# Optimization experiments

Hardware: AMD Instinct MI355X
Metric: run time of the kernel (lower is better)

The kernel has to match this reference:

```python
import jax, jax.numpy as jnp
import numpy as np

B, S, T, H, NH, NL = 16, 128, 64, 128, 8, 4
DH = H // NH
FF = 2 * H
SCALE = 1.0 / float(np.sqrt(DH))


def _ln(x, s, b):
    m = x.mean(-1, keepdims=True)
    v = ((x - m) ** 2).mean(-1, keepdims=True)
    return (x - m) * jax.lax.rsqrt(v + 1e-5) * s + b


def _block(x, mask, p):
    Wq, bq, Wk, bk, Wv, bv, Wo, bo, s1, c1, W1, d1, W2, d2, s2, c2 = p
    N, L, _ = x.shape
    q = (x @ Wq + bq).reshape(N, L, NH, DH)
    k = (x @ Wk + bk).reshape(N, L, NH, DH)
    v = (x @ Wv + bv).reshape(N, L, NH, DH)
    scores = jnp.einsum('nqhd,nkhd->nhqk', q, k) * SCALE
    scores = jnp.where(mask[:, None, :, :], scores, -1e9)
    a = jax.nn.softmax(scores, axis=-1)
    o = jnp.einsum('nhqk,nkhd->nqhd', a, v).reshape(N, L, H)
    x = _ln(x + o @ Wo + bo, s1, c1)
    h = jax.nn.relu(x @ W1 + d1)
    return _ln(x + h @ W2 + d2, s2, c2)


def setup_inputs():
    key = jax.random.key(0)
    ks = jax.random.split(key, 16)
    g = lambda k, shape: jax.random.normal(k, shape, jnp.float32) * 0.02
    return {
        'polylines': jax.random.normal(ks[0], (B, S, T, H), jnp.float32),
        'lengths': jax.random.randint(ks[1], (B, S), 0, T + 1),
        'proj_w': g(ks[2], (H, H)), 'proj_b': jnp.zeros((H,), jnp.float32),
        'proj_ln_s': jnp.ones((H,), jnp.float32), 'proj_ln_b': jnp.zeros((H,), jnp.float32),
        'pos_emb': g(ks[3], (1, T, H)),
        'Wq': g(ks[4], (NL, H, H)), 'bq': jnp.zeros((NL, H), jnp.float32),
        'Wk': g(ks[5], (NL, H, H)), 'bk': jnp.zeros((NL, H), jnp.float32),
        'Wv': g(ks[6], (NL, H, H)), 'bv': jnp.zeros((NL, H), jnp.float32),
        'Wo': g(ks[7], (NL, H, H)), 'bo': jnp.zeros((NL, H), jnp.float32),
        'ln1_s': jnp.ones((NL, H), jnp.float32), 'ln1_b': jnp.zeros((NL, H), jnp.float32),
        'W1': g(ks[8], (NL, H, FF)), 'b1': jnp.zeros((NL, FF), jnp.float32),
        'W2': g(ks[9], (NL, FF, H)), 'b2': jnp.zeros((NL, H), jnp.float32),
        'ln2_s': jnp.ones((NL, H), jnp.float32), 'ln2_b': jnp.zeros((NL, H), jnp.float32),
    }


def reference(polylines, lengths, proj_w, proj_b, proj_ln_s, proj_ln_b, pos_emb,
              Wq, bq, Wk, bk, Wv, bv, Wo, bo, ln1_s, ln1_b, W1, b1, W2, b2, ln2_s, ln2_b):
    # valid[b,s,t] = t < lengths[b,s]; lengths==0 -> polyline absent (fully padded)
    valid = jnp.arange(T)[None, None, :] < lengths[:, :, None]  # [B,S,T]
    x = jnp.where(valid[..., None], polylines, -1.0)            # -1 pad as in np.pad(constant_values=-1)
    # mask_temporal[b,s] = outer(valid[b,s], valid[b,s])
    mask_t = (valid[:, :, :, None] & valid[:, :, None, :]).reshape(B * S, T, T)
    # mask_spatial[b,t] = outer(valid[b,:,t], valid[b,:,t])
    vs = jnp.transpose(valid, (0, 2, 1))                        # [B,T,S]
    mask_s = (vs[:, :, :, None] & vs[:, :, None, :]).reshape(B * T, S, S)

    x = x.reshape(B * S, T, H)
    x = jax.nn.relu(_ln(x @ proj_w + proj_b, proj_ln_s, proj_ln_b))  # MLP: Linear->LN->ReLU
    x = x + pos_emb[:, :T, :]

    mask = mask_t
    for i in range(NL):
        if i == NL // 2:
            # switch from temporal to spatial attention: [B*S,T,H] -> [B*T,S,H]
            x = x.reshape(B, S, T, H).transpose(0, 2, 1, 3).reshape(B * T, S, H)
            mask = mask_s
        p = (Wq[i], bq[i], Wk[i], bk[i], Wv[i], bv[i], Wo[i], bo[i],
             ln1_s[i], ln1_b[i], W1[i], b1[i], W2[i], b2[i], ln2_s[i], ln2_b[i])
        x = _block(x, mask, p)
    # faithful to original final reshape (treats [B*T,S,H] buffer as [B,S,T,H])
    return x.reshape(B, S, T, H)[:, 0, :]
```

## Files before the change

kernel.cpp:

```cpp
#include <hip/hip_runtime.h>

typedef short short8 __attribute__((ext_vector_type(8)));
typedef short short4_t __attribute__((ext_vector_type(4)));
typedef float floatx4 __attribute__((ext_vector_type(4)));
typedef unsigned short ushort_t;

#define B_ 16
#define S_ 128
#define T_ 64
#define H_ 128
#define FF_ 256
#define SCALEQK 0.25f

#define EPI_BIAS 0
#define EPI_RELU 1
#define EPI_LNRES 2
#define EPI_PROJ 3

#define OFFP 0
#define OFFQ(l) (16384 + (l) * 65536)
#define OFFK(l) (OFFQ(l) + 16384)
#define OFFV(l) (OFFQ(l) + 32768)
#define OFFO(l) (OFFQ(l) + 49152)
#define OFFW1(l) (278528 + (l) * 65536)
#define OFFW2(l) (OFFW1(l) + 32768)

__device__ __forceinline__ float b2f(ushort_t u) {
    union { unsigned int i; float f; } x; x.i = ((unsigned int)u) << 16; return x.f;
}
__device__ __forceinline__ ushort_t f2b(float f) {
    union { float f; unsigned int i; } x; x.f = f;
    unsigned int r = x.i + 0x7fffu + ((x.i >> 16) & 1u);
    return (ushort_t)(r >> 16);
}
__device__ __forceinline__ int pack2b(float a, float b) {
    return (int)f2b(a) | ((int)f2b(b) << 16);
}

struct WtEnt { const float* src; int N; int K; int nclog2; int dstoff; };
struct WtArgs { WtEnt e[25]; };

__global__ __launch_bounds__(256) void wt_kernel(WtArgs a, ushort_t* __restrict__ dst) {
    WtEnt ent = a.e[blockIdx.x];
    const int tiles_c = ent.N >> 5;
    const int nt = (ent.K >> 5) * tiles_c;
    const int t = blockIdx.y;
    if (t >= nt) return;
    const int tc = t & (tiles_c - 1);
    const int tr = t >> ent.nclog2;
    __shared__ float ld[32 * 33];
    const int tid = threadIdx.x;
#pragma unroll
    for (int i = 0; i < 4; ++i) {
        int e = tid + i * 256;
        int rr = e >> 5, cc = e & 31;
        ld[rr * 33 + cc] = ent.src[(tr * 32 + rr) * ent.N + tc * 32 + cc];
    }
    __syncthreads();
    ushort_t* d = dst + ent.dstoff;
#pragma unroll
    for (int i = 0; i < 4; ++i) {
        int e = tid + i * 256;
        int rr = e >> 5, cc = e & 31;
        d[(tc * 32 + rr) * ent.K + tr * 32 + cc] = f2b(ld[cc * 33 + rr]);
    }
}

template<int K, int EPI, bool PAD, bool FINAL, bool MULTI, bool OUTB, bool AB16>
__global__ __launch_bounds__(256, 2) void gemm_mfma(
    const void* __restrict__ Av, int lda,
    const ushort_t* wt0, const ushort_t* wt1, const ushort_t* wt2,
    const float* b0, const float* b1, const float* b2,
    const float* __restrict__ resid, int rstride,
    const float* __restrict__ lns, const float* __restrict__ lnb,
    const float* __restrict__ pos, const int* __restrict__ lens,
    void* o0, void* o1, void* o2,
    int Ntot)
{
    __shared__ ushort_t aL[128 * 136];
    __shared__ ushort_t wL[128 * 136];

    const int tid = threadIdx.x;
    const int lane = tid & 63, wv = tid >> 6;
    const size_t rowbase = (size_t)blockIdx.x * 128;

    const ushort_t* wT; const float* bias; void* out; int cbase;
    if (MULTI) {
        int sel = blockIdx.y;
        wT = sel == 0 ? wt0 : (sel == 1 ? wt1 : wt2);
        bias = sel == 0 ? b0 : (sel == 1 ? b1 : b2);
        out = sel == 0 ? o0 : (sel == 1 ? o1 : o2);
        cbase = 0;
    } else {
        wT = wt0; bias = b0; out = o0; cbase = blockIdx.y * 128;
    }

    floatx4 acc[2][8];
#pragma unroll
    for (int a = 0; a < 2; ++a)
#pragma unroll
        for (int c = 0; c < 8; ++c) acc[a][c] = (floatx4){0.f, 0.f, 0.f, 0.f};

    const int arow = wv * 32 + (lane & 15);
    const int koff = (lane >> 4) * 8;

    for (int kc = 0; kc < K; kc += 128) {
        if (kc) __syncthreads();
#pragma unroll
        for (int it = 0; it < 8; ++it) {
            int e8 = tid + it * 256;
            int row = e8 >> 4, kg = e8 & 15;
            int kk = kc + kg * 8;
            short8 val;
            if (AB16) {
                val = *(const short8*)((const ushort_t*)Av + (size_t)(rowbase + row) * lda + kk);
            } else {
                const float* Af = (const float*)Av + (size_t)(rowbase + row) * lda + kk;
                float f[8];
                *(float4*)(f) = *(const float4*)(Af);
                *(float4*)(f + 4) = *(const float4*)(Af + 4);
                if (PAD) {
                    int r = (int)(rowbase + row);
                    if ((r & 63) >= lens[r >> 6]) {
#pragma unroll
                        for (int q = 0; q < 8; ++q) f[q] = -1.0f;
                    }
                }
#pragma unroll
                for (int q = 0; q < 8; ++q) val[q] = (short)f2b(f[q]);
            }
            *(short8*)&aL[row * 136 + kg * 8] = val;
        }
#pragma unroll
        for (int it = 0; it < 8; ++it) {
            int e8 = tid + it * 256;
            int n = e8 >> 4, kg = e8 & 15;
            *(short8*)&wL[n * 136 + kg * 8] =
                *(const short8*)&wT[(size_t)(cbase + n) * K + kc + kg * 8];
        }
        __syncthreads();
#pragma unroll
        for (int k0 = 0; k0 < 128; k0 += 32) {
            short8 a0 = *(const short8*)&aL[arow * 136 + k0 + koff];
            short8 a1 = *(const short8*)&aL[(arow + 16) * 136 + k0 + koff];
#pragma unroll
            for (int ct = 0; ct < 8; ++ct) {
                short8 b = *(const short8*)&wL[(ct * 16 + (lane & 15)) * 136 + k0 + koff];
                acc[0][ct] = __builtin_amdgcn_mfma_f32_16x16x32_bf16(a0, b, acc[0][ct], 0, 0, 0);
                acc[1][ct] = __builtin_amdgcn_mfma_f32_16x16x32_bf16(a1, b, acc[1][ct], 0, 0, 0);
            }
        }
    }

    const int col16 = lane & 15;
    const int rgrp = (lane >> 4) * 4;
    float bcol[8], lnsc[8], lnbc[8];
#pragma unroll
    for (int ct = 0; ct < 8; ++ct) bcol[ct] = bias[cbase + ct * 16 + col16];
    if (EPI == EPI_LNRES || EPI == EPI_PROJ) {
#pragma unroll
        for (int ct = 0; ct < 8; ++ct) {
            lnsc[ct] = lns[ct * 16 + col16];
            lnbc[ct] = lnb[ct * 16 + col16];
        }
    }

#pragma unroll
    for (int rt = 0; rt < 2; ++rt) {
        const int rbase = wv * 32 + rt * 16 + rgrp;
#pragma unroll
        for (int ct = 0; ct < 8; ++ct)
#pragma unroll
            for (int rg = 0; rg < 4; ++rg) {
                float v = acc[rt][ct][rg] + bcol[ct];
                if (EPI == EPI_LNRES)
                    v += resid[(rowbase + rbase + rg) * (size_t)rstride + ct * 16 + col16];
                acc[rt][ct][rg] = v;
            }
        if (EPI == EPI_LNRES || EPI == EPI_PROJ) {
            float mean[4], rstd[4];
#pragma unroll
            for (int rg = 0; rg < 4; ++rg) {
                float s = 0.f;
#pragma unroll
                for (int ct = 0; ct < 8; ++ct) s += acc[rt][ct][rg];
                s += __shfl_xor(s, 1); s += __shfl_xor(s, 2);
                s += __shfl_xor(s, 4); s += __shfl_xor(s, 8);
                mean[rg] = s * (1.f / 128.f);
            }
#pragma unroll
            for (int rg = 0; rg < 4; ++rg) {
                float s = 0.f;
#pragma unroll
                for (int ct = 0; ct < 8; ++ct) {
                    float d = acc[rt][ct][rg] - mean[rg];
                    s += d * d;
                }
                s += __shfl_xor(s, 1); s += __shfl_xor(s, 2);
                s += __shfl_xor(s, 4); s += __shfl_xor(s, 8);
                rstd[rg] = rsqrtf(s * (1.f / 128.f) + 1e-5f);
            }
#pragma unroll
            for (int ct = 0; ct < 8; ++ct)
#pragma unroll
                for (int rg = 0; rg < 4; ++rg)
                    acc[rt][ct][rg] = (acc[rt][ct][rg] - mean[rg]) * rstd[rg] * lnsc[ct] + lnbc[ct];
        }
#pragma unroll
        for (int ct = 0; ct < 8; ++ct)
#pragma unroll
            for (int rg = 0; rg < 4; ++rg) {
                size_t grow = rowbase + rbase + rg;
                int col = cbase + ct * 16 + col16;
                float v = acc[rt][ct][rg];
                if (EPI == EPI_RELU) v = fmaxf(v, 0.f);
                if (EPI == EPI_PROJ)
                    v = fmaxf(v, 0.f) + pos[((int)grow & 63) * H_ + ct * 16 + col16];
                if (FINAL) {
                    int b = (int)(grow >> 7), s = (int)(grow & 127);
                    if (s < T_) ((float*)out)[((size_t)(b * T_ + s)) * H_ + col] = v;
                } else if (OUTB) {
                    ((ushort_t*)out)[grow * (size_t)Ntot + col] = f2b(v);
                } else {
                    ((float*)out)[grow * (size_t)Ntot + col] = v;
                }
            }
    }
}

__global__ __launch_bounds__(256, 1) void attn_s(
    ushort_t* qo, const ushort_t* __restrict__ kk, const ushort_t* __restrict__ vv,
    const int* __restrict__ lens)
{
    __shared__ float kL[128 * 36];
    __shared__ float vL[128 * 36];
    __shared__ int vldL[128];
    const int tid = threadIdx.x;
    const int b = blockIdx.x, hp = blockIdx.y;
    const size_t rowg = (size_t)b * 128;

    if (tid < 128) vldL[tid] = (lens[b * 128 + tid] > 0) ? 1 : 0;
#pragma unroll
    for (int it = 0; it < 2; ++it) {
        int e8 = tid + it * 256;
        int j = e8 >> 2, dg = e8 & 3;
        short8 k8 = *(const short8*)&kk[(rowg + j) * 128 + hp * 32 + dg * 8];
        short8 v8 = *(const short8*)&vv[(rowg + j) * 128 + hp * 32 + dg * 8];
        float* kd = &kL[j * 36 + dg * 8];
        float* vd = &vL[j * 36 + dg * 8];
#pragma unroll
        for (int q = 0; q < 8; ++q) { kd[q] = b2f((ushort_t)k8[q]); vd[q] = b2f((ushort_t)v8[q]); }
    }
    __syncthreads();

    const int hl = tid >> 7;
    const int i = tid & 127;
    const int hc = hl * 16;
    const int h = hp * 2 + hl;

    float qf[16];
    {
        const short8* qp = (const short8*)&qo[(rowg + i) * 128 + h * 16];
        short8 q0 = qp[0], q1 = qp[1];
#pragma unroll
        for (int q = 0; q < 8; ++q) { qf[q] = b2f((ushort_t)q0[q]); qf[8 + q] = b2f((ushort_t)q1[q]); }
    }

    float sc[128];
    const bool iv = vldL[i] != 0;
#pragma unroll
    for (int j = 0; j < 128; ++j) {
        const float* kr = &kL[j * 36 + hc];
        float s = 0.f;
#pragma unroll
        for (int d = 0; d < 16; ++d) s = fmaf(qf[d], kr[d], s);
        sc[j] = (iv && vldL[j]) ? s * SCALEQK : -1e9f;
    }
    float m = -3.0e38f;
#pragma unroll
    for (int j = 0; j < 128; ++j) m = fmaxf(m, sc[j]);
    float sum = 0.f;
#pragma unroll
    for (int j = 0; j < 128; ++j) { float e = __expf(sc[j] - m); sc[j] = e; sum += e; }
    const float inv = 1.0f / sum;
    float of[16];
#pragma unroll
    for (int d = 0; d < 16; ++d) of[d] = 0.f;
#pragma unroll
    for (int j = 0; j < 128; ++j) {
        float p = sc[j] * inv;
        const float* vr = &vL[j * 36 + hc];
#pragma unroll
        for (int d = 0; d < 16; ++d) of[d] = fmaf(p, vr[d], of[d]);
    }
    short8 o0v, o1v;
#pragma unroll
    for (int q = 0; q < 8; ++q) { o0v[q] = (short)f2b(of[q]); o1v[q] = (short)f2b(of[8 + q]); }
    short8* op = (short8*)&qo[(rowg + i) * 128 + h * 16];
    op[0] = o0v; op[1] = o1v;
}

template<int RT, int CT, int KK>
__device__ __forceinline__ void mm_g(const ushort_t* aL, int sa,
                                     const ushort_t* __restrict__ wT,
                                     int colbase, int lane, floatx4 (&acc)[RT][CT]) {
    const int l15 = lane & 15, lq8 = (lane >> 4) * 8;
#pragma unroll
    for (int r = 0; r < RT; ++r)
#pragma unroll
        for (int c = 0; c < CT; ++c) acc[r][c] = (floatx4){0.f, 0.f, 0.f, 0.f};
#pragma unroll
    for (int k0 = 0; k0 < KK; k0 += 32) {
        short8 b[CT];
#pragma unroll
        for (int c = 0; c < CT; ++c)
            b[c] = *(const short8*)&wT[(colbase + c * 16 + l15) * KK + k0 + lq8];
#pragma unroll
        for (int r = 0; r < RT; ++r) {
            short8 a = *(const short8*)&aL[(r * 16 + l15) * sa + k0 + lq8];
#pragma unroll
            for (int c = 0; c < CT; ++c)
                acc[r][c] = __builtin_amdgcn_mfma_f32_16x16x32_bf16(a, b[c], acc[r][c], 0, 0, 0);
        }
    }
}

template<int RT, int CT>
__device__ __forceinline__ void add_bias(floatx4 (&acc)[RT][CT], const float* b,
                                         int colbase, int l15) {
#pragma unroll
    for (int c = 0; c < CT; ++c) {
        float bc = b[colbase + c * 16 + l15];
#pragma unroll
        for (int r = 0; r < RT; ++r)
#pragma unroll
            for (int g = 0; g < 4; ++g) acc[r][c][g] += bc;
    }
}

template<int RT, int CT>
__device__ __forceinline__ void add_resid_reg(floatx4 (&acc)[RT][CT],
                                              const float (&res)[RT][CT][4]) {
#pragma unroll
    for (int r = 0; r < RT; ++r)
#pragma unroll
        for (int c = 0; c < CT; ++c)
#pragma unroll
            for (int g = 0; g < 4; ++g) acc[r][c][g] += res[r][c][g];
}
template<int RT, int CT>
__device__ __forceinline__ void save_resid(float (&res)[RT][CT][4],
                                           const floatx4 (&acc)[RT][CT]) {
#pragma unroll
    for (int r = 0; r < RT; ++r)
#pragma unroll
        for (int c = 0; c < CT; ++c)
#pragma unroll
            for (int g = 0; g < 4; ++g) res[r][c][g] = acc[r][c][g];
}

template<int RT, int CT>
__device__ __forceinline__ void st_n(const floatx4 (&acc)[RT][CT], ushort_t* dst, int stride,
                                     int colbase, int l15, int lq) {
#pragma unroll
    for (int r = 0; r < RT; ++r)
#pragma unroll
        for (int g = 0; g < 4; ++g) {
            int row = r * 16 + lq * 4 + g;
#pragma unroll
            for (int c = 0; c < CT; ++c)
                dst[row * stride + colbase + c * 16 + l15] = f2b(acc[r][c][g]);
        }
}

template<int RT, int CT>
__device__ __forceinline__ void st_t(const floatx4 (&acc)[RT][CT], ushort_t* dst, int stride,
                                     int colbase, int l15, int lq) {
#pragma unroll
    for (int r = 0; r < RT; ++r)
#pragma unroll
        for (int c = 0; c < CT; ++c) {
            int d = colbase + c * 16 + l15;
            short4_t p;
#pragma unroll
            for (int g = 0; g < 4; ++g) p[g] = (short)f2b(acc[r][c][g]);
            *(short4_t*)&dst[d * stride + r * 16 + lq * 4] = p;
        }
}

template<int RT, int CT>
__device__ __forceinline__ void ln_norm(floatx4 (&acc)[RT][CT], float* redL,
                                        const float* lns, const float* lnb,
                                        int colbase, int l15, int lq, int wv) {
#pragma unroll
    for (int r = 0; r < RT; ++r)
#pragma unroll
        for (int g = 0; g < 4; ++g) {
            float s = 0.f, q = 0.f;
#pragma unroll
            for (int c = 0; c < CT; ++c) { float v = acc[r][c][g]; s += v; q += v * v; }
            s += __shfl_xor(s, 1); s += __shfl_xor(s, 2); s += __shfl_xor(s, 4); s += __shfl_xor(s, 8);
            q += __shfl_xor(q, 1); q += __shfl_xor(q, 2); q += __shfl_xor(q, 4); q += __shfl_xor(q, 8);
            if (l15 == 0) {
                int row = r * 16 + lq * 4 + g;
                redL[row * 8 + wv] = s;
                redL[row * 8 + 4 + wv] = q;
            }
        }
    __syncthreads();
#pragma unroll
    for (int r = 0; r < RT; ++r)
#pragma unroll
        for (int g = 0; g < 4; ++g) {
            int row = r * 16 + lq * 4 + g;
            float4 S = *(float4*)&redL[row * 8];
            float4 Q = *(float4*)&redL[row * 8 + 4];
            float mean = (S.x + S.y + S.z + S.w) * (1.f / 128.f);
            float var = (Q.x + Q.y + Q.z + Q.w) * (1.f / 128.f) - mean * mean;
            float rstd = rsqrtf(var + 1e-5f);
#pragma unroll
            for (int c = 0; c < CT; ++c) {
                int col = colbase + c * 16 + l15;
                acc[r][c][g] = (acc[r][c][g] - mean) * rstd * lns[col] + lnb[col];
            }
        }
}

template<int JT>
__device__ __forceinline__ void softmax_pack(floatx4 (&st)[JT], bool iv, unsigned jm,
                                             int (&px)[JT][2]) {
    float ev[JT][4];
    float mx = -3.0e38f;
#pragma unroll
    for (int jt = 0; jt < JT; ++jt)
#pragma unroll
        for (int g = 0; g < 4; ++g) {
            bool ok = iv && ((jm >> (jt * 4 + g)) & 1u);
            float s = ok ? st[jt][g] * SCALEQK : -1e9f;
            ev[jt][g] = s; mx = fmaxf(mx, s);
        }
    mx = fmaxf(mx, __shfl_xor(mx, 16)); mx = fmaxf(mx, __shfl_xor(mx, 32));
    float sum = 0.f;
#pragma unroll
    for (int jt = 0; jt < JT; ++jt)
#pragma unroll
        for (int g = 0; g < 4; ++g) { float e = __expf(ev[jt][g] - mx); ev[jt][g] = e; sum += e; }
    sum += __shfl_xor(sum, 16); sum += __shfl_xor(sum, 32);
    float inv = 1.f / sum;
#pragma unroll
    for (int jt = 0; jt < JT; ++jt) {
        px[jt][0] = pack2b(ev[jt][0] * inv, ev[jt][1] * inv);
        px[jt][1] = pack2b(ev[jt][2] * inv, ev[jt][3] * inv);
    }
}

__device__ __forceinline__ short8 pfrag(const int (*px)[2], int jc, int lq, int l15) {
    const int jA = (lq & 1) * 32 + l15;
    int a0 = __shfl(px[jc * 2][0], jA);
    int a1 = __shfl(px[jc * 2][1], jA);
    int a2 = __shfl(px[jc * 2][0], jA + 16);
    int a3 = __shfl(px[jc * 2][1], jA + 16);
    int b0 = __shfl(px[jc * 2 + 1][0], jA);
    int b1 = __shfl(px[jc * 2 + 1][1], jA);
    int b2 = __shfl(px[jc * 2 + 1][0], jA + 16);
    int b3 = __shfl(px[jc * 2 + 1][1], jA + 16);
    const bool t = (lq >> 1) != 0;
    union { int4 i; short8 s; } u;
    u.i = make_int4(t ? b0 : a0, t ? b1 : a1, t ? b2 : a2, t ? b3 : a3);
    return u.s;
}
__device__ __forceinline__ short8 vfrag(const ushort_t* vT, int stride, int row, int off) {
    int2 a = *(const int2*)&vT[row * stride + off];
    int2 b = *(const int2*)&vT[row * stride + off + 4];
    union { int4 i; short8 s; } u;
    u.i = make_int4(a.x, a.y, b.x, b.y);
    return u.s;
}

__global__ __launch_bounds__(256, 2) void k1_mega(
    const float* __restrict__ poly, const int* __restrict__ lens,
    const ushort_t* __restrict__ wt,
    const float* __restrict__ projb, const float* __restrict__ pls,
    const float* __restrict__ plb, const float* __restrict__ pos,
    const float* __restrict__ bq0, const float* __restrict__ bk0,
    const float* __restrict__ bv0, const float* __restrict__ bo0,
    const float* __restrict__ l1s0, const float* __restrict__ l1b0,
    const float* __restrict__ b10, const float* __restrict__ b20,
    const float* __restrict__ l2s0, const float* __restrict__ l2b0,
    const float* __restrict__ bq1, const float* __restrict__ bk1,
    const float* __restrict__ bv1,
    ushort_t* __restrict__ o1, float* __restrict__ xr0f)
{
    __shared__ ushort_t pool[34816];
    __shared__ float redL[512];
    __shared__ float psL[8 * 68];
    __shared__ float q1L[128];
    ushort_t* xL = pool;
    ushort_t* qL = pool + 8704;
    ushort_t* kL = pool + 17408;
    ushort_t* vT = pool + 26112;
    ushort_t* hL = pool + 17408;

    const int tid = threadIdx.x, lane = tid & 63, wv = tid >> 6;
    const int l15 = lane & 15, lq = lane >> 4;
    const int gid = blockIdx.x;
    const int len = lens[gid];

    {
        const float* pg = poly + (size_t)gid * 8192;
#pragma unroll
        for (int it = 0; it < 8; ++it) {
            int e4 = (tid + it * 256) * 4;
            int row = e4 >> 7, col = e4 & 127;
            float4 f = *(const float4*)(pg + e4);
            if (row >= len) { f.x = -1.f; f.y = -1.f; f.z = -1.f; f.w = -1.f; }
            short4_t u;
            u[0] = (short)f2b(f.x); u[1] = (short)f2b(f.y);
            u[2] = (short)f2b(f.z); u[3] = (short)f2b(f.w);
            *(short4_t*)&xL[row * 136 + col] = u;
        }
    }
    __syncthreads();

    floatx4 a2[4][2];
    float xre[4][2][4];

    mm_g<4, 2, 128>(xL, 136, wt + OFFP, wv * 32, lane, a2);
    add_bias<4, 2>(a2, projb, wv * 32, l15);
    ln_norm<4, 2>(a2, redL, pls, plb, wv * 32, l15, lq, wv);
    __syncthreads();
#pragma unroll
    for (int r = 0; r < 4; ++r)
#pragma unroll
        for (int gg = 0; gg < 4; ++gg) {
            int row = r * 16 + lq * 4 + gg;
#pragma unroll
            for (int c = 0; c < 2; ++c) {
                int col = wv * 32 + c * 16 + l15;
                float v = fmaxf(a2[r][c][gg], 0.f) + pos[row * 128 + col];
                xre[r][c][gg] = v;
                xL[row * 136 + col] = f2b(v);
            }
        }
    __syncthreads();

    mm_g<4, 2, 128>(xL, 136, wt + OFFQ(0), wv * 32, lane, a2);
    add_bias<4, 2>(a2, bq0, wv * 32, l15);
    st_n<4, 2>(a2, qL, 136, wv * 32, l15, lq);
    mm_g<4, 2, 128>(xL, 136, wt + OFFK(0), wv * 32, lane, a2);
    add_bias<4, 2>(a2, bk0, wv * 32, l15);
    st_n<4, 2>(a2, kL, 136, wv * 32, l15, lq);
    mm_g<4, 2, 128>(xL, 136, wt + OFFV(0), wv * 32, lane, a2);
    add_bias<4, 2>(a2, bv0, wv * 32, l15);
    st_t<4, 2>(a2, vT, 68, wv * 32, l15, lq);
    __syncthreads();

    {
        const int iRow = wv * 16 + l15;
        const bool iv = iRow < len;
        unsigned jm = 0;
#pragma unroll
        for (int jt = 0; jt < 4; ++jt)
#pragma unroll
            for (int gg = 0; gg < 4; ++gg)
                if (jt * 16 + lq * 4 + gg < len) jm |= (1u << (jt * 4 + gg));
        for (int h = 0; h < 8; ++h) {
            const int hc = h * 16;
            short8 z8 = {0, 0, 0, 0, 0, 0, 0, 0};
            short8 bqf = z8;
            if (lq < 2) bqf = *(const short8*)&qL[iRow * 136 + hc + lq * 8];
            floatx4 st[4];
#pragma unroll
            for (int jt = 0; jt < 4; ++jt) {
                short8 ak = z8;
                if (lq < 2) ak = *(const short8*)&kL[(jt * 16 + l15) * 136 + hc + lq * 8];
                floatx4 zz = {0.f, 0.f, 0.f, 0.f};
                st[jt] = __builtin_amdgcn_mfma_f32_16x16x32_bf16(ak, bqf, zz, 0, 0, 0);
            }
            int px[4][2];
            softmax_pack<4>(st, iv, jm, px);
            floatx4 ao = {0.f, 0.f, 0.f, 0.f};
#pragma unroll
            for (int jc = 0; jc < 2; ++jc) {
                short8 av = vfrag(vT, 68, hc + l15, jc * 32 + lq * 8);
                short8 bp = pfrag(px, jc, lq, l15);
                ao = __builtin_amdgcn_mfma_f32_16x16x32_bf16(av, bp, ao, 0, 0, 0);
            }
            short4_t w;
#pragma unroll
            for (int gg = 0; gg < 4; ++gg) w[gg] = (short)f2b(ao[gg]);
            *(short4_t*)&qL[iRow * 136 + hc + lq * 4] = w;
        }
    }
    __syncthreads();

    mm_g<4, 2, 128>(qL, 136, wt + OFFO(0), wv * 32, lane, a2);
    add_bias<4, 2>(a2, bo0, wv * 32, l15);
    add_resid_reg<4, 2>(a2, xre);
    ln_norm<4, 2>(a2, redL, l1s0, l1b0, wv * 32, l15, lq, wv);
    save_resid<4, 2>(xre, a2);
    st_n<4, 2>(a2, xL, 136, wv * 32, l15, lq);
    __syncthreads();

    {
        floatx4 a4[4][4];
        mm_g<4, 4, 128>(xL, 136, wt + OFFW1(0), wv * 64, lane, a4);
        add_bias<4, 4>(a4, b10, wv * 64, l15);
#pragma unroll
        for (int r = 0; r < 4; ++r)
#pragma unroll
            for (int c = 0; c < 4; ++c)
#pragma unroll
                for (int gg = 0; gg < 4; ++gg) a4[r][c][gg] = fmaxf(a4[r][c][gg], 0.f);
        st_n<4, 4>(a4, hL, 272, wv * 64, l15, lq);
    }
    __syncthreads();

    mm_g<4, 2, 256>(hL, 272, wt + OFFW2(0), wv * 32, lane, a2);
    add_bias<4, 2>(a2, b20, wv * 32, l15);
    add_resid_reg<4, 2>(a2, xre);
    ln_norm<4, 2>(a2, redL, l2s0, l2b0, wv * 32, l15, lq, wv);
    save_resid<4, 2>(xre, a2);
    st_n<4, 2>(a2, xL, 136, wv * 32, l15, lq);
    if (lq == 0) {
#pragma unroll
        for (int c = 0; c < 2; ++c)
            xr0f[(size_t)gid * 128 + wv * 32 + c * 16 + l15] = a2[0][c][0];
    }
    __syncthreads();

    mm_g<4, 2, 128>(xL, 136, wt + OFFK(1), wv * 32, lane, a2);
    add_bias<4, 2>(a2, bk1, wv * 32, l15);
    st_n<4, 2>(a2, kL, 136, wv * 32, l15, lq);
    mm_g<4, 2, 128>(xL, 136, wt + OFFV(1), wv * 32, lane, a2);
    add_bias<4, 2>(a2, bv1, wv * 32, l15);
    st_t<4, 2>(a2, vT, 68, wv * 32, l15, lq);
    if (tid < 128) {
        int d = tid;
        float a = bq1[d];
        const ushort_t* wq = wt + OFFQ(1) + d * 128;
#pragma unroll 4
        for (int j0 = 0; j0 < 128; j0 += 8) {
            short8 w8 = *(const short8*)&wq[j0];
            short8 x8 = *(const short8*)&xL[j0];
#pragma unroll
            for (int q = 0; q < 8; ++q)
                a = fmaf(b2f((ushort_t)x8[q]), b2f((ushort_t)w8[q]), a);
        }
        q1L[d] = a;
    }
    __syncthreads();

    {
        int h = tid >> 5, jj = tid & 31;
        int hc = h * 16;
        float s[2];
#pragma unroll
        for (int half = 0; half < 2; ++half) {
            int j = jj + half * 32;
            float a = 0.f;
            short8 k0v = *(const short8*)&kL[j * 136 + hc];
            short8 k1v = *(const short8*)&kL[j * 136 + hc + 8];
#pragma unroll
            for (int q = 0; q < 8; ++q) {
                a = fmaf(q1L[hc + q], b2f((ushort_t)k0v[q]), a);
                a = fmaf(q1L[hc + 8 + q], b2f((ushort_t)k1v[q]), a);
            }
            s[half] = (j < len) ? a * SCALEQK : -1e9f;
        }
        float mx = fmaxf(s[0], s[1]);
#pragma unroll
        for (int d = 1; d < 32; d <<= 1) mx = fmaxf(mx, __shfl_xor(mx, d));
        float e0 = __expf(s[0] - mx), e1 = __expf(s[1] - mx);
        float sum = e0 + e1;
#pragma unroll
        for (int d = 1; d < 32; d <<= 1) sum += __shfl_xor(sum, d);
        float inv = 1.f / sum;
        psL[h * 68 + jj] = e0 * inv;
        psL[h * 68 + jj + 32] = e1 * inv;
    }
    __syncthreads();
    if (tid < 128) {
        int h = tid >> 4, d = tid & 15, hc = h * 16;
        float a = 0.f;
#pragma unroll 4
        for (int j0 = 0; j0 < 64; j0 += 4) {
            float4 p4 = *(const float4*)&psL[h * 68 + j0];
            short4_t v4 = *(const short4_t*)&vT[(hc + d) * 68 + j0];
            a += p4.x * b2f((ushort_t)v4[0]) + p4.y * b2f((ushort_t)v4[1])
               + p4.z * b2f((ushort_t)v4[2]) + p4.w * b2f((ushort_t)v4[3]);
        }
        o1[(size_t)gid * 128 + hc + d] = f2b(a);
    }
}

extern "C" void kernel_launch(void* const* d_in, const int* in_sizes, int n_in,
                              void* d_out, int out_size, void* d_ws, size_t ws_size,
                              hipStream_t stream)
{
    const float* poly   = (const float*)d_in[0];
    const int*   lens   = (const int*)d_in[1];
    const float* proj_w = (const float*)d_in[2];
    const float* proj_b = (const float*)d_in[3];
    const float* pls    = (const float*)d_in[4];
    const float* plb    = (const float*)d_in[5];
    const float* pos    = (const float*)d_in[6];
    const float* Wq = (const float*)d_in[7];
    const float* bq = (const float*)d_in[8];
    const float* Wk = (const float*)d_in[9];
    const float* bk = (const float*)d_in[10];
    const float* Wv = (const float*)d_in[11];
    const float* bv = (const float*)d_in[12];
    const float* Wo = (const float*)d_in[13];
    const float* bo = (const float*)d_in[14];
    const float* l1s = (const float*)d_in[15];
    const float* l1b = (const float*)d_in[16];
    const float* W1 = (const float*)d_in[17];
    const float* b1 = (const float*)d_in[18];
    const float* W2 = (const float*)d_in[19];
    const float* b2 = (const float*)d_in[20];
    const float* l2s = (const float*)d_in[21];
    const float* l2b = (const float*)d_in[22];
    float* outp = (float*)d_out;

    char* base = (char*)d_ws;
    ushort_t* wt    = (ushort_t*)base;
    ushort_t* o1buf = (ushort_t*)(base + 1081344);
    float* xr0f     = (float*)(base + 1605632);
    float* ybuf     = (float*)(base + 2654208);
    ushort_t* hsml  = (ushort_t*)(base + 3702784);
    ushort_t* q2    = (ushort_t*)(base + 4751360);
    ushort_t* k2b   = (ushort_t*)(base + 5275648);
    ushort_t* v2    = (ushort_t*)(base + 5799936);

    const int HH = H_ * H_, HF = H_ * FF_;
    WtArgs wa;
    wa.e[0] = {proj_w, 128, 128, 2, OFFP};
    for (int l = 0; l < 4; ++l) {
        wa.e[1 + l * 4 + 0] = {Wq + l * HH, 128, 128, 2, OFFQ(l)};
        wa.e[1 + l * 4 + 1] = {Wk + l * HH, 128, 128, 2, OFFK(l)};
        wa.e[1 + l * 4 + 2] = {Wv + l * HH, 128, 128, 2, OFFV(l)};
        wa.e[1 + l * 4 + 3] = {Wo + l * HH, 128, 128, 2, OFFO(l)};
    }
    for (int l = 0; l < 4; ++l) {
        wa.e[17 + l * 2 + 0] = {W1 + l * HF, 256, 128, 3, OFFW1(l)};
        wa.e[17 + l * 2 + 1] = {W2 + l * HF, 128, 256, 2, OFFW2(l)};
    }
    wt_kernel<<<dim3(25, 32), 256, 0, stream>>>(wa, wt);

    k1_mega<<<dim3(2048), 256, 0, stream>>>(
        poly, lens, wt,
        proj_b, pls, plb, pos,
        bq, bk, bv, bo, l1s, l1b, b1, b2, l2s, l2b,
        bq + H_, bk + H_, bv + H_,
        o1buf, xr0f);

    gemm_mfma<128, EPI_LNRES, false, false, false, false, true><<<dim3(16, 1), 256, 0, stream>>>(
        o1buf, 128, wt + OFFO(1), wt + OFFO(1), wt + OFFO(1), bo + H_, bo + H_, bo + H_,
        xr0f, 128, l1s + H_, l1b + H_, nullptr, nullptr, ybuf, ybuf, ybuf, H_);
    gemm_mfma<128, EPI_RELU, false, false, false, true, false><<<dim3(16, 2), 256, 0, stream>>>(
        ybuf, 128, wt + OFFW1(1), wt + OFFW1(1), wt + OFFW1(1), b1 + FF_, b1 + FF_, b1 + FF_,
        nullptr, 0, nullptr, nullptr, nullptr, nullptr, hsml, hsml, hsml, FF_);
    gemm_mfma<256, EPI_LNRES, false, false, false, false, true><<<dim3(16, 1), 256, 0, stream>>>(
        hsml, 256, wt + OFFW2(1), wt + OFFW2(1), wt + OFFW2(1), b2 + H_, b2 + H_, b2 + H_,
        ybuf, 128, l2s + H_, l2b + H_, nullptr, nullptr, ybuf, ybuf, ybuf, H_);

    for (int l = 2; l < 4; ++l) {
        gemm_mfma<128, EPI_BIAS, false, false, true, true, false><<<dim3(16, 3), 256, 0, stream>>>(
            ybuf, 128, wt + OFFQ(l), wt + OFFK(l), wt + OFFV(l),
            bq + l * H_, bk + l * H_, bv + l * H_,
            nullptr, 0, nullptr, nullptr, nullptr, nullptr, q2, k2b, v2, H_);
        attn_s<<<dim3(16, 4), 256, 0, stream>>>(q2, k2b, v2, lens);
        gemm_mfma<128, EPI_LNRES, false, false, false, false, true><<<dim3(16, 1), 256, 0, stream>>>(
            q2, 128, wt + OFFO(l), wt + OFFO(l), wt + OFFO(l), bo + l * H_, bo + l * H_, bo + l * H_,
            ybuf, 128, l1s + l * H_, l1b + l * H_, nullptr, nullptr, ybuf, ybuf, ybuf, H_);
        gemm_mfma<128, EPI_RELU, false, false, false, true, false><<<dim3(16, 2), 256, 0, stream>>>(
            ybuf, 128, wt + OFFW1(l), wt + OFFW1(l), wt + OFFW1(l),
            b1 + l * FF_, b1 + l * FF_, b1 + l * FF_,
            nullptr, 0, nullptr, nullptr, nullptr, nullptr, hsml, hsml, hsml, FF_);
        if (l < 3) {
            gemm_mfma<256, EPI_LNRES, false, false, false, false, true><<<dim3(16, 1), 256, 0, stream>>>(
                hsml, 256, wt + OFFW2(l), wt + OFFW2(l), wt + OFFW2(l),
                b2 + l * H_, b2 + l * H_, b2 + l * H_,
                ybuf, 128, l2s + l * H_, l2b + l * H_, nullptr, nullptr, ybuf, ybuf, ybuf, H_);
        } else {
            gemm_mfma<256, EPI_LNRES, false, true, false, false, true><<<dim3(16, 1), 256, 0, stream>>>(
                hsml, 256, wt + OFFW2(l), wt + OFFW2(l), wt + OFFW2(l),
                b2 + l * H_, b2 + l * H_, b2 + l * H_,
                ybuf, 128, l2s + l * H_, l2b + l * H_, nullptr, nullptr, outp, outp, outp, H_);
        }
    }
}
```

Baseline: 431.5 us.

## Fuse remaining transformer layers into single per-batch megakernel with MFMA attention

Replaces the chain of separate GEMM and spatial attention launches for layers 1-3 with one kernel, one block per batch, that keeps activations in shared memory and residuals in registers. Attention is now computed with MFMA instructions instead of scalar FMAs. This removes many kernel launches and the global round trips of intermediate buffers. The cost is that only 16 blocks run, so the work that previously spread over more blocks now has far less parallelism.

```diff
diff --git a/kernel.cpp b/kernel.cpp
--- a/kernel.cpp
+++ b/kernel.cpp
@@ -11,11 +11,6 @@
 #define H_ 128
 #define FF_ 256
 #define SCALEQK 0.25f
-
-#define EPI_BIAS 0
-#define EPI_RELU 1
-#define EPI_LNRES 2
-#define EPI_PROJ 3
 
 #define OFFP 0
 #define OFFQ(l) (16384 + (l) * 65536)
@@ -64,240 +59,6 @@
         int rr = e >> 5, cc = e & 31;
         d[(tc * 32 + rr) * ent.K + tr * 32 + cc] = f2b(ld[cc * 33 + rr]);
     }
-}
-
-template<int K, int EPI, bool PAD, bool FINAL, bool MULTI, bool OUTB, bool AB16>
-__global__ __launch_bounds__(256, 2) void gemm_mfma(
-    const void* __restrict__ Av, int lda,
-    const ushort_t* wt0, const ushort_t* wt1, const ushort_t* wt2,
-    const float* b0, const float* b1, const float* b2,
-    const float* __restrict__ resid, int rstride,
-    const float* __restrict__ lns, const float* __restrict__ lnb,
-    const float* __restrict__ pos, const int* __restrict__ lens,
-    void* o0, void* o1, void* o2,
-    int Ntot)
-{
-    __shared__ ushort_t aL[128 * 136];
-    __shared__ ushort_t wL[128 * 136];
-
-    const int tid = threadIdx.x;
-    const int lane = tid & 63, wv = tid >> 6;
-    const size_t rowbase = (size_t)blockIdx.x * 128;
-
-    const ushort_t* wT; const float* bias; void* out; int cbase;
-    if (MULTI) {
-        int sel = blockIdx.y;
-        wT = sel == 0 ? wt0 : (sel == 1 ? wt1 : wt2);
-        bias = sel == 0 ? b0 : (sel == 1 ? b1 : b2);
-        out = sel == 0 ? o0 : (sel == 1 ? o1 : o2);
-        cbase = 0;
-    } else {
-        wT = wt0; bias = b0; out = o0; cbase = blockIdx.y * 128;
-    }
-
-    floatx4 acc[2][8];
-#pragma unroll
-    for (int a = 0; a < 2; ++a)
-#pragma unroll
-        for (int c = 0; c < 8; ++c) acc[a][c] = (floatx4){0.f, 0.f, 0.f, 0.f};
-
-    const int arow = wv * 32 + (lane & 15);
-    const int koff = (lane >> 4) * 8;
-
-    for (int kc = 0; kc < K; kc += 128) {
-        if (kc) __syncthreads();
-#pragma unroll
-        for (int it = 0; it < 8; ++it) {
-            int e8 = tid + it * 256;
-            int row = e8 >> 4, kg = e8 & 15;
-            int kk = kc + kg * 8;
-            short8 val;
-            if (AB16) {
-                val = *(const short8*)((const ushort_t*)Av + (size_t)(rowbase + row) * lda + kk);
-            } else {
-                const float* Af = (const float*)Av + (size_t)(rowbase + row) * lda + kk;
-                float f[8];
-                *(float4*)(f) = *(const float4*)(Af);
-                *(float4*)(f + 4) = *(const float4*)(Af + 4);
-                if (PAD) {
-                    int r = (int)(rowbase + row);
-                    if ((r & 63) >= lens[r >> 6]) {
-#pragma unroll
-                        for (int q = 0; q < 8; ++q) f[q] = -1.0f;
-                    }
-                }
-#pragma unroll
-                for (int q = 0; q < 8; ++q) val[q] = (short)f2b(f[q]);
-            }
-            *(short8*)&aL[row * 136 + kg * 8] = val;
-        }
-#pragma unroll
-        for (int it = 0; it < 8; ++it) {
-            int e8 = tid + it * 256;
-            int n = e8 >> 4, kg = e8 & 15;
-            *(short8*)&wL[n * 136 + kg * 8] =
-                *(const short8*)&wT[(size_t)(cbase + n) * K + kc + kg * 8];
-        }
-        __syncthreads();
-#pragma unroll
-        for (int k0 = 0; k0 < 128; k0 += 32) {
-            short8 a0 = *(const short8*)&aL[arow * 136 + k0 + koff];
-            short8 a1 = *(const short8*)&aL[(arow + 16) * 136 + k0 + koff];
-#pragma unroll
-            for (int ct = 0; ct < 8; ++ct) {
-                short8 b = *(const short8*)&wL[(ct * 16 + (lane & 15)) * 136 + k0 + koff];
-                acc[0][ct] = __builtin_amdgcn_mfma_f32_16x16x32_bf16(a0, b, acc[0][ct], 0, 0, 0);
-                acc[1][ct] = __builtin_amdgcn_mfma_f32_16x16x32_bf16(a1, b, acc[1][ct], 0, 0, 0);
-            }
-        }
-    }
-
-    const int col16 = lane & 15;
-    const int rgrp = (lane >> 4) * 4;
-    float bcol[8], lnsc[8], lnbc[8];
-#pragma unroll
-    for (int ct = 0; ct < 8; ++ct) bcol[ct] = bias[cbase + ct * 16 + col16];
-    if (EPI == EPI_LNRES || EPI == EPI_PROJ) {
-#pragma unroll
-        for (int ct = 0; ct < 8; ++ct) {
-            lnsc[ct] = lns[ct * 16 + col16];
-            lnbc[ct] = lnb[ct * 16 + col16];
-        }
-    }
-
-#pragma unroll
-    for (int rt = 0; rt < 2; ++rt) {
-        const int rbase = wv * 32 + rt * 16 + rgrp;
-#pragma unroll
-        for (int ct = 0; ct < 8; ++ct)
-#pragma unroll
-            for (int rg = 0; rg < 4; ++rg) {
-                float v = acc[rt][ct][rg] + bcol[ct];
-                if (EPI == EPI_LNRES)
-                    v += resid[(rowbase + rbase + rg) * (size_t)rstride + ct * 16 + col16];
-                acc[rt][ct][rg] = v;
-            }
-        if (EPI == EPI_LNRES || EPI == EPI_PROJ) {
-            float mean[4], rstd[4];
-#pragma unroll
-            for (int rg = 0; rg < 4; ++rg) {
-                float s = 0.f;
-#pragma unroll
-                for (int ct = 0; ct < 8; ++ct) s += acc[rt][ct][rg];
-                s += __shfl_xor(s, 1); s += __shfl_xor(s, 2);
-                s += __shfl_xor(s, 4); s += __shfl_xor(s, 8);
-                mean[rg] = s * (1.f / 128.f);
-            }
-#pragma unroll
-            for (int rg = 0; rg < 4; ++rg) {
-                float s = 0.f;
-#pragma unroll
-                for (int ct = 0; ct < 8; ++ct) {
-                    float d = acc[rt][ct][rg] - mean[rg];
-                    s += d * d;
-                }
-                s += __shfl_xor(s, 1); s += __shfl_xor(s, 2);
-                s += __shfl_xor(s, 4); s += __shfl_xor(s, 8);
-                rstd[rg] = rsqrtf(s * (1.f / 128.f) + 1e-5f);
-            }
-#pragma unroll
-            for (int ct = 0; ct < 8; ++ct)
-#pragma unroll
-                for (int rg = 0; rg < 4; ++rg)
-                    acc[rt][ct][rg] = (acc[rt][ct][rg] - mean[rg]) * rstd[rg] * lnsc[ct] + lnbc[ct];
-        }
-#pragma unroll
-        for (int ct = 0; ct < 8; ++ct)
-#pragma unroll
-            for (int rg = 0; rg < 4; ++rg) {
-                size_t grow = rowbase + rbase + rg;
-                int col = cbase + ct * 16 + col16;
-                float v = acc[rt][ct][rg];
-                if (EPI == EPI_RELU) v = fmaxf(v, 0.f);
-                if (EPI == EPI_PROJ)
-                    v = fmaxf(v, 0.f) + pos[((int)grow & 63) * H_ + ct * 16 + col16];
-                if (FINAL) {
-                    int b = (int)(grow >> 7), s = (int)(grow & 127);
-                    if (s < T_) ((float*)out)[((size_t)(b * T_ + s)) * H_ + col] = v;
-                } else if (OUTB) {
-                    ((ushort_t*)out)[grow * (size_t)Ntot + col] = f2b(v);
-                } else {
-                    ((float*)out)[grow * (size_t)Ntot + col] = v;
-                }
-            }
-    }
-}
-
-__global__ __launch_bounds__(256, 1) void attn_s(
-    ushort_t* qo, const ushort_t* __restrict__ kk, const ushort_t* __restrict__ vv,
-    const int* __restrict__ lens)
-{
-    __shared__ float kL[128 * 36];
-    __shared__ float vL[128 * 36];
-    __shared__ int vldL[128];
-    const int tid = threadIdx.x;
-    const int b = blockIdx.x, hp = blockIdx.y;
-    const size_t rowg = (size_t)b * 128;
-
-    if (tid < 128) vldL[tid] = (lens[b * 128 + tid] > 0) ? 1 : 0;
-#pragma unroll
-    for (int it = 0; it < 2; ++it) {
-        int e8 = tid + it * 256;
-        int j = e8 >> 2, dg = e8 & 3;
-        short8 k8 = *(const short8*)&kk[(rowg + j) * 128 + hp * 32 + dg * 8];
-        short8 v8 = *(const short8*)&vv[(rowg + j) * 128 + hp * 32 + dg * 8];
-        float* kd = &kL[j * 36 + dg * 8];
-        float* vd = &vL[j * 36 + dg * 8];
-#pragma unroll
-        for (int q = 0; q < 8; ++q) { kd[q] = b2f((ushort_t)k8[q]); vd[q] = b2f((ushort_t)v8[q]); }
-    }
-    __syncthreads();
-
-    const int hl = tid >> 7;
-    const int i = tid & 127;
-    const int hc = hl * 16;
-    const int h = hp * 2 + hl;
-
-    float qf[16];
-    {
-        const short8* qp = (const short8*)&qo[(rowg + i) * 128 + h * 16];
-        short8 q0 = qp[0], q1 = qp[1];
-#pragma unroll
-        for (int q = 0; q < 8; ++q) { qf[q] = b2f((ushort_t)q0[q]); qf[8 + q] = b2f((ushort_t)q1[q]); }
-    }
-
-    float sc[128];
-    const bool iv = vldL[i] != 0;
-#pragma unroll
-    for (int j = 0; j < 128; ++j) {
-        const float* kr = &kL[j * 36 + hc];
-        float s = 0.f;
-#pragma unroll
-        for (int d = 0; d < 16; ++d) s = fmaf(qf[d], kr[d], s);
-        sc[j] = (iv && vldL[j]) ? s * SCALEQK : -1e9f;
-    }
-    float m = -3.0e38f;
-#pragma unroll
-    for (int j = 0; j < 128; ++j) m = fmaxf(m, sc[j]);
-    float sum = 0.f;
-#pragma unroll
-    for (int j = 0; j < 128; ++j) { float e = __expf(sc[j] - m); sc[j] = e; sum += e; }
-    const float inv = 1.0f / sum;
-    float of[16];
-#pragma unroll
-    for (int d = 0; d < 16; ++d) of[d] = 0.f;
-#pragma unroll
-    for (int j = 0; j < 128; ++j) {
-        float p = sc[j] * inv;
-        const float* vr = &vL[j * 36 + hc];
-#pragma unroll
-        for (int d = 0; d < 16; ++d) of[d] = fmaf(p, vr[d], of[d]);
-    }
-    short8 o0v, o1v;
-#pragma unroll
-    for (int q = 0; q < 8; ++q) { o0v[q] = (short)f2b(of[q]); o1v[q] = (short)f2b(of[8 + q]); }
-    short8* op = (short8*)&qo[(rowg + i) * 128 + h * 16];
-    op[0] = o0v; op[1] = o1v;
 }
 
 template<int RT, int CT, int KK>
@@ -691,6 +452,149 @@
                + p4.z * b2f((ushort_t)v4[2]) + p4.w * b2f((ushort_t)v4[3]);
         }
         o1[(size_t)gid * 128 + hc + d] = f2b(a);
+    }
+}
+
+__global__ __launch_bounds__(256, 1) void k2_mega(
+    const ushort_t* __restrict__ o1, const float* __restrict__ xr0f,
+    const int* __restrict__ lens, const ushort_t* __restrict__ wt,
+    const float* __restrict__ bq, const float* __restrict__ bk,
+    const float* __restrict__ bv, const float* __restrict__ bo,
+    const float* __restrict__ l1s, const float* __restrict__ l1b,
+    const float* __restrict__ b1, const float* __restrict__ b2,
+    const float* __restrict__ l2s, const float* __restrict__ l2b,
+    float* __restrict__ outp)
+{
+    __shared__ ushort_t pool[69632];
+    __shared__ float redL[1024];
+    __shared__ int vldL[128];
+    ushort_t* xL = pool;
+    ushort_t* qL = pool + 17408;
+    ushort_t* kL = pool + 34816;
+    ushort_t* vT = pool + 52224;
+    ushort_t* hL = pool + 34816;
+
+    const int tid = threadIdx.x, lane = tid & 63, wv = tid >> 6;
+    const int l15 = lane & 15, lq = lane >> 4;
+    const int b = blockIdx.x;
+    const size_t rowg = (size_t)b * 128;
+
+#pragma unroll
+    for (int it = 0; it < 8; ++it) {
+        int e8 = tid + it * 256;
+        int row = e8 >> 4, kg = e8 & 15;
+        *(short8*)&xL[row * 136 + kg * 8] = *(const short8*)&o1[(rowg + row) * 128 + kg * 8];
+    }
+    if (tid < 128) vldL[tid] = (lens[b * 128 + tid] > 0) ? 1 : 0;
+    __syncthreads();
+
+    unsigned jm = 0;
+#pragma unroll
+    for (int jt = 0; jt < 8; ++jt)
+#pragma unroll
+        for (int g = 0; g < 4; ++g)
+            if (vldL[jt * 16 + lq * 4 + g]) jm |= (1u << (jt * 4 + g));
+
+    float xre[8][2][4];
+#pragma unroll
+    for (int r = 0; r < 8; ++r)
+#pragma unroll
+        for (int c = 0; c < 2; ++c)
+#pragma unroll
+            for (int g = 0; g < 4; ++g)
+                xre[r][c][g] = xr0f[(rowg + r * 16 + lq * 4 + g) * 128 + wv * 32 + c * 16 + l15];
+
+    floatx4 a2[8][2];
+
+    for (int l = 1; l < 4; ++l) {
+        if (l >= 2) {
+            mm_g<8, 2, 128>(xL, 136, wt + OFFQ(l), wv * 32, lane, a2);
+            add_bias<8, 2>(a2, bq + l * H_, wv * 32, l15);
+            st_n<8, 2>(a2, qL, 136, wv * 32, l15, lq);
+            mm_g<8, 2, 128>(xL, 136, wt + OFFK(l), wv * 32, lane, a2);
+            add_bias<8, 2>(a2, bk + l * H_, wv * 32, l15);
+            st_n<8, 2>(a2, kL, 136, wv * 32, l15, lq);
+            mm_g<8, 2, 128>(xL, 136, wt + OFFV(l), wv * 32, lane, a2);
+            add_bias<8, 2>(a2, bv + l * H_, wv * 32, l15);
+            st_t<8, 2>(a2, vT, 136, wv * 32, l15, lq);
+            __syncthreads();
+            for (int h = 0; h < 8; ++h) {
+                const int hc = h * 16;
+#pragma unroll
+                for (int iblk = 0; iblk < 2; ++iblk) {
+                    const int iRow = iblk * 64 + wv * 16 + l15;
+                    const bool iv = vldL[iRow] != 0;
+                    short8 z8 = {0, 0, 0, 0, 0, 0, 0, 0};
+                    short8 bqf = z8;
+                    if (lq < 2) bqf = *(const short8*)&qL[iRow * 136 + hc + lq * 8];
+                    floatx4 st[8];
+#pragma unroll
+                    for (int jt = 0; jt < 8; ++jt) {
+                        short8 ak = z8;
+                        if (lq < 2) ak = *(const short8*)&kL[(jt * 16 + l15) * 136 + hc + lq * 8];
+                        floatx4 zz = {0.f, 0.f, 0.f, 0.f};
+                        st[jt] = __builtin_amdgcn_mfma_f32_16x16x32_bf16(ak, bqf, zz, 0, 0, 0);
+                    }
+                    int px[8][2];
+                    softmax_pack<8>(st, iv, jm, px);
+                    floatx4 ao = {0.f, 0.f, 0.f, 0.f};
+#pragma unroll
+                    for (int jc = 0; jc < 4; ++jc) {
+                        short8 av = vfrag(vT, 136, hc + l15, jc * 32 + lq * 8);
+                        short8 bp = pfrag(px, jc, lq, l15);
+                        ao = __builtin_amdgcn_mfma_f32_16x16x32_bf16(av, bp, ao, 0, 0, 0);
+                    }
+                    short4_t w;
+#pragma unroll
+                    for (int g = 0; g < 4; ++g) w[g] = (short)f2b(ao[g]);
+                    *(short4_t*)&qL[iRow * 136 + hc + lq * 4] = w;
+                }
+            }
+            __syncthreads();
+        }
+
+        const ushort_t* aIn = (l == 1) ? xL : qL;
+        mm_g<8, 2, 128>(aIn, 136, wt + OFFO(l), wv * 32, lane, a2);
+        add_bias<8, 2>(a2, bo + l * H_, wv * 32, l15);
+        add_resid_reg<8, 2>(a2, xre);
+        ln_norm<8, 2>(a2, redL, l1s + l * H_, l1b + l * H_, wv * 32, l15, lq, wv);
+        save_resid<8, 2>(xre, a2);
+        st_n<8, 2>(a2, xL, 136, wv * 32, l15, lq);
+        __syncthreads();
+
+        {
+            floatx4 a4[8][4];
+            mm_g<8, 4, 128>(xL, 136, wt + OFFW1(l), wv * 64, lane, a4);
+            add_bias<8, 4>(a4, b1 + l * FF_, wv * 64, l15);
+#pragma unroll
+            for (int r = 0; r < 8; ++r)
+#pragma unroll
+                for (int c = 0; c < 4; ++c)
+#pragma unroll
+                    for (int g = 0; g < 4; ++g) a4[r][c][g] = fmaxf(a4[r][c][g], 0.f);
+            st_n<8, 4>(a4, hL, 272, wv * 64, l15, lq);
+        }
+        __syncthreads();
+
+        mm_g<8, 2, 256>(hL, 272, wt + OFFW2(l), wv * 32, lane, a2);
+        add_bias<8, 2>(a2, b2 + l * H_, wv * 32, l15);
+        add_resid_reg<8, 2>(a2, xre);
+        ln_norm<8, 2>(a2, redL, l2s + l * H_, l2b + l * H_, wv * 32, l15, lq, wv);
+        if (l == 3) {
+#pragma unroll
+            for (int r = 0; r < 4; ++r)
+#pragma unroll
+                for (int c = 0; c < 2; ++c)
+#pragma unroll
+                    for (int g = 0; g < 4; ++g) {
+                        int row = r * 16 + lq * 4 + g;
+                        outp[((size_t)(b * 64 + row)) * 128 + wv * 32 + c * 16 + l15] = a2[r][c][g];
+                    }
+        } else {
+            save_resid<8, 2>(xre, a2);
+            st_n<8, 2>(a2, xL, 136, wv * 32, l15, lq);
+            __syncthreads();
+        }
     }
 }
 
@@ -727,11 +631,6 @@
     ushort_t* wt    = (ushort_t*)base;
     ushort_t* o1buf = (ushort_t*)(base + 1081344);
     float* xr0f     = (float*)(base + 1605632);
-    float* ybuf     = (float*)(base + 2654208);
-    ushort_t* hsml  = (ushort_t*)(base + 3702784);
-    ushort_t* q2    = (ushort_t*)(base + 4751360);
-    ushort_t* k2b   = (ushort_t*)(base + 5275648);
-    ushort_t* v2    = (ushort_t*)(base + 5799936);
 
     const int HH = H_ * H_, HF = H_ * FF_;
     WtArgs wa;
@@ -755,39 +654,8 @@
         bq + H_, bk + H_, bv + H_,
         o1buf, xr0f);
 
-    gemm_mfma<128, EPI_LNRES, false, false, false, false, true><<<dim3(16, 1), 256, 0, stream>>>(
-        o1buf, 128, wt + OFFO(1), wt + OFFO(1), wt + OFFO(1), bo + H_, bo + H_, bo + H_,
-        xr0f, 128, l1s + H_, l1b + H_, nullptr, nullptr, ybuf, ybuf, ybuf, H_);
-    gemm_mfma<128, EPI_RELU, false, false, false, true, false><<<dim3(16, 2), 256, 0, stream>>>(
-        ybuf, 128, wt + OFFW1(1), wt + OFFW1(1), wt + OFFW1(1), b1 + FF_, b1 + FF_, b1 + FF_,
-        nullptr, 0, nullptr, nullptr, nullptr, nullptr, hsml, hsml, hsml, FF_);
-    gemm_mfma<256, EPI_LNRES, false, false, false, false, true><<<dim3(16, 1), 256, 0, stream>>>(
-        hsml, 256, wt + OFFW2(1), wt + OFFW2(1), wt + OFFW2(1), b2 + H_, b2 + H_, b2 + H_,
-        ybuf, 128, l2s + H_, l2b + H_, nullptr, nullptr, ybuf, ybuf, ybuf, H_);
-
-    for (int l = 2; l < 4; ++l) {
-        gemm_mfma<128, EPI_BIAS, false, false, true, true, false><<<dim3(16, 3), 256, 0, stream>>>(
-            ybuf, 128, wt + OFFQ(l), wt + OFFK(l), wt + OFFV(l),
-            bq + l * H_, bk + l * H_, bv + l * H_,
-            nullptr, 0, nullptr, nullptr, nullptr, nullptr, q2, k2b, v2, H_);
-        attn_s<<<dim3(16, 4), 256, 0, stream>>>(q2, k2b, v2, lens);
-        gemm_mfma<128, EPI_LNRES, false, false, false, false, true><<<dim3(16, 1), 256, 0, stream>>>(
-            q2, 128, wt + OFFO(l), wt + OFFO(l), wt + OFFO(l), bo + l * H_, bo + l * H_, bo + l * H_,
-            ybuf, 128, l1s + l * H_, l1b + l * H_, nullptr, nullptr, ybuf, ybuf, ybuf, H_);
-        gemm_mfma<128, EPI_RELU, false, false, false, true, false><<<dim3(16, 2), 256, 0, stream>>>(
-            ybuf, 128, wt + OFFW1(l), wt + OFFW1(l), wt + OFFW1(l),
-            b1 + l * FF_, b1 + l * FF_, b1 + l * FF_,
-            nullptr, 0, nullptr, nullptr, nullptr, nullptr, hsml, hsml, hsml, FF_);
-        if (l < 3) {
-            gemm_mfma<256, EPI_LNRES, false, false, false, false, true><<<dim3(16, 1), 256, 0, stream>>>(
-                hsml, 256, wt + OFFW2(l), wt + OFFW2(l), wt + OFFW2(l),
-                b2 + l * H_, b2 + l * H_, b2 + l * H_,
-                ybuf, 128, l2s + l * H_, l2b + l * H_, nullptr, nullptr, ybuf, ybuf, ybuf, H_);
-        } else {
-            gemm_mfma<256, EPI_LNRES, false, true, false, false, true><<<dim3(16, 1), 256, 0, stream>>>(
-                hsml, 256, wt + OFFW2(l), wt + OFFW2(l), wt + OFFW2(l),
-                b2 + l * H_, b2 + l * H_, b2 + l * H_,
-                ybuf, 128, l2s + l * H_, l2b + l * H_, nullptr, nullptr, outp, outp, outp, H_);
-        }
-    }
-}
+    k2_mega<<<dim3(16), 256, 0, stream>>>(
+        o1buf, xr0f, lens, wt,
+        bq, bk, bv, bo, l1s, l1b, b1, b2, l2s, l2b,
+        outp);
+}
```

Measured after the change: 474.6 us. 1.1x slower.
